# Optimization experiments

Measured on AMD Instinct MI355X. Metric: run time of the kernel, lower is better.

Reference implementation:

```python
import jax, jax.numpy as jnp
import numpy as np

N_HEADS = 16
D_K = 64
DIM = 1024
NEG = -1e12
LN_EPS = 1e-5


def setup_inputs() -> dict:
    key = jax.random.key(0)
    ks = jax.random.split(key, 8)
    B, S, D = 2, 2048, DIM
    H, K = N_HEADS, D_K
    f = lambda k, shp: jax.random.normal(k, shp, dtype=jnp.float32)
    scale = 0.02
    return {
        "input_Q": f(ks[0], (B, S, D)),
        "input_K": f(ks[1], (B, S, D)),
        "input_V": f(ks[2], (B, S, D)),
        "attention_mask": jax.random.randint(ks[3], (B, S), 0, 2, dtype=jnp.int32),
        "W_Q": f(ks[4], (H * K, D)) * scale,  # nn.Linear weight layout [out, in]
        "W_K": f(ks[5], (H * K, D)) * scale,
        "W_V": f(ks[6], (H * K, D)) * scale,
        "W_O": f(ks[7], (D, H * K)) * scale,
        "gamma": jnp.ones((D,), jnp.float32),
        "beta": jnp.zeros((D,), jnp.float32),
    }


def reference(input_Q, input_K, input_V, attention_mask, W_Q, W_K, W_V, W_O, gamma, beta):
    B, S, D = input_Q.shape

    def proj(x, W):  # [B,S,D] @ [HK,D]^T -> [B,H,S,K]
        return (x @ W.T).reshape(B, S, N_HEADS, D_K).transpose(0, 2, 1, 3)

    Q = proj(input_Q, W_Q)
    K = proj(input_K, W_K)
    V = proj(input_V, W_V)

    scores = jnp.einsum('bhqk,bhsk->bhqs', Q, K) / np.float32(np.sqrt(D_K))

    # Faithful reproduction of scores_mask (including its inverted-looking logic):
    # mask = clamp(padding_mask + strict_upper_tri - 1, min=0); scores += (1-mask)*NEG
    am = attention_mask.astype(scores.dtype)[:, None, None, :]          # [B,1,1,S]
    low_tri = jnp.triu(jnp.ones((S, S), scores.dtype), k=1)             # 1 - tril(ones)
    m = jnp.maximum(am + low_tri - 1.0, 0.0)
    scores = scores + (1.0 - m) * NEG

    attn = jax.nn.softmax(scores, axis=-1)
    ctx = jnp.einsum('bhqs,bhsk->bhqk', attn, V)                        # [B,H,S,K]
    ctx = ctx.transpose(0, 2, 1, 3).reshape(B, S, N_HEADS * D_K)

    out = ctx @ W_O.T + input_Q                                         # fc + residual
    mu = jnp.mean(out, axis=-1, keepdims=True)
    var = jnp.var(out, axis=-1, keepdims=True)
    return (out - mu) / jnp.sqrt(var + LN_EPS) * gamma + beta
```

## Files before the change

### kernel.cpp

```cpp
#include <hip/hip_runtime.h>

#define NH    16
#define DK    64
#define DIM   1024
#define BATCH 2
#define SEQ   2048
#define MROWS (BATCH*SEQ)
#define QSCALE 0.18033688011112043f
#define SENT   -44.0f
#define PCONST 5.684341886080802e-14f

typedef unsigned short bfraw;
typedef __attribute__((ext_vector_type(8))) __bf16 bf16x8;
typedef __attribute__((ext_vector_type(4))) __bf16 bf16x4;
typedef __attribute__((ext_vector_type(8))) unsigned short u16x8;
typedef __attribute__((ext_vector_type(4))) unsigned short u16x4;
typedef __attribute__((ext_vector_type(4))) short s16x4;
typedef __attribute__((ext_vector_type(4))) float f32x4;

__device__ __forceinline__ float bf2f(bfraw u) {
    union { unsigned int i; float f; } x; x.i = ((unsigned int)u) << 16; return x.f;
}
__device__ __forceinline__ bfraw f2bf(float f) {
    union { float f; unsigned int i; } x; x.f = f;
    unsigned int r = x.i + 0x7FFFu + ((x.i >> 16) & 1u);
    return (bfraw)(r >> 16);
}
__device__ __forceinline__ bfraw f2bf_trunc(float f) {
    union { float f; unsigned int i; } x; x.f = f;
    return (bfraw)(x.i >> 16);
}
__device__ __forceinline__ float fexp2(float x) {
#if __has_builtin(__builtin_amdgcn_exp2f)
    return __builtin_amdgcn_exp2f(x);
#else
    return exp2f(x);
#endif
}

__device__ __forceinline__ f32x4 mfma16(s16x4 a, s16x4 b, f32x4 c) {
#if __has_builtin(__builtin_amdgcn_mfma_f32_16x16x16_bf16)
    union { s16x4 s; bf16x4 h; } ua, ub; ua.s = a; ub.s = b;
    return __builtin_amdgcn_mfma_f32_16x16x16_bf16(ua.h, ub.h, c, 0, 0, 0);
#elif __has_builtin(__builtin_amdgcn_mfma_f32_16x16x16bf16_1k)
    return __builtin_amdgcn_mfma_f32_16x16x16bf16_1k(a, b, c, 0, 0, 0);
#else
    asm("v_mfma_f32_16x16x16_bf16 %0, %1, %2, %0" : "+v"(c) : "v"(a), "v"(b));
    return c;
#endif
}

__device__ __forceinline__ float block_reduce(float val, float* rbuf, int op) {
    const int lane = threadIdx.x & 63, wave = threadIdx.x >> 6;
    #pragma unroll
    for (int off = 32; off; off >>= 1) {
        float o = __shfl_xor(val, off, 64);
        val = op ? (val + o) : fmaxf(val, o);
    }
    if (lane == 0) rbuf[wave] = val;
    __syncthreads();
    float r = op ? (rbuf[0] + rbuf[1] + rbuf[2] + rbuf[3])
                 : fmaxf(fmaxf(rbuf[0], rbuf[1]), fmaxf(rbuf[2], rbuf[3]));
    __syncthreads();
    return r;
}

__global__ __launch_bounds__(256) void cvt_kernel(
        const float* __restrict__ x0, const float* __restrict__ x1, const float* __restrict__ x2,
        const float* __restrict__ w0, const float* __restrict__ w1, const float* __restrict__ w2,
        const float* __restrict__ w3, bfraw* __restrict__ Xb, bfraw* __restrict__ Wb) {
    const int t = blockIdx.y;
    const float* src; bfraw* dst; int n;
    if (t < 3) { src = (t == 0) ? x0 : (t == 1) ? x1 : x2; dst = Xb + t * (MROWS * DIM); n = MROWS * DIM; }
    else { int u = t - 3; src = (u == 0) ? w0 : (u == 1) ? w1 : (u == 2) ? w2 : w3;
           dst = Wb + u * (DIM * DIM); n = DIM * DIM; }
    int idx = (blockIdx.x * 256 + threadIdx.x) * 8;
    if (idx >= n) return;
    f32x4 a = *(const f32x4*)(src + idx);
    f32x4 b = *(const f32x4*)(src + idx + 4);
    u16x8 o;
    #pragma unroll
    for (int j = 0; j < 4; j++) { o[j] = f2bf(a[j]); o[4 + j] = f2bf(b[j]); }
    *(u16x8*)(dst + idx) = o;
}

__device__ __forceinline__ void gemm128(const bfraw* __restrict__ A, const bfraw* __restrict__ B,
                                        int m0, int n0, f32x4 acc[4][4]) {
    __shared__ __align__(16) bfraw As[128 * 64];
    __shared__ __align__(16) bfraw Bs[128 * 64];
    const int tid = threadIdx.x, wave = tid >> 6;
    const int lane = tid & 63, lrow = lane & 15, quad = lane >> 4;
    const int wy = wave >> 1, wx = wave & 1;
    const int swz = lrow & 7;
    const int srow = tid >> 2;
    const int cg0  = (tid & 3) << 1;
    const int gc   = cg0 << 3;
    const int e7   = srow & 7;
    const int o0 = ((cg0 ^ e7) << 3), o1 = (((cg0 | 1) ^ e7) << 3);

    u16x8 ha[4], hb[4];
    const bfraw* pa0 = A + (m0 + srow) * DIM + gc;
    const bfraw* pa1 = A + (m0 + 64 + srow) * DIM + gc;
    const bfraw* pb0 = B + (n0 + srow) * DIM + gc;
    const bfraw* pb1 = B + (n0 + 64 + srow) * DIM + gc;

    #pragma unroll
    for (int i = 0; i < 4; i++)
        #pragma unroll
        for (int j = 0; j < 4; j++) { f32x4 z = {0.f, 0.f, 0.f, 0.f}; acc[i][j] = z; }

    ha[0] = *(const u16x8*)(pa0);     ha[1] = *(const u16x8*)(pa0 + 8);
    ha[2] = *(const u16x8*)(pa1);     ha[3] = *(const u16x8*)(pa1 + 8);
    hb[0] = *(const u16x8*)(pb0);     hb[1] = *(const u16x8*)(pb0 + 8);
    hb[2] = *(const u16x8*)(pb1);     hb[3] = *(const u16x8*)(pb1 + 8);

    for (int k0 = 0; k0 < DIM; k0 += 64) {
        __syncthreads();
        *(u16x8*)&As[srow * 64 + o0]        = ha[0];
        *(u16x8*)&As[srow * 64 + o1]        = ha[1];
        *(u16x8*)&As[(64 + srow) * 64 + o0] = ha[2];
        *(u16x8*)&As[(64 + srow) * 64 + o1] = ha[3];
        *(u16x8*)&Bs[srow * 64 + o0]        = hb[0];
        *(u16x8*)&Bs[srow * 64 + o1]        = hb[1];
        *(u16x8*)&Bs[(64 + srow) * 64 + o0] = hb[2];
        *(u16x8*)&Bs[(64 + srow) * 64 + o1] = hb[3];
        __syncthreads();
        if (k0 + 64 < DIM) {
            const int k1 = k0 + 64;
            ha[0] = *(const u16x8*)(pa0 + k1);     ha[1] = *(const u16x8*)(pa0 + k1 + 8);
            ha[2] = *(const u16x8*)(pa1 + k1);     ha[3] = *(const u16x8*)(pa1 + k1 + 8);
            hb[0] = *(const u16x8*)(pb0 + k1);     hb[1] = *(const u16x8*)(pb0 + k1 + 8);
            hb[2] = *(const u16x8*)(pb1 + k1);     hb[3] = *(const u16x8*)(pb1 + k1 + 8);
        }
        #pragma unroll
        for (int ks = 0; ks < 2; ks++) {
            const int c = (ks << 2) | quad;
            bf16x8 af[4], bfg[4];
            #pragma unroll
            for (int mi = 0; mi < 4; mi++)
                af[mi] = *(const bf16x8*)&As[(wy * 64 + mi * 16 + lrow) * 64 + ((c ^ swz) << 3)];
            #pragma unroll
            for (int ni = 0; ni < 4; ni++)
                bfg[ni] = *(const bf16x8*)&Bs[(wx * 64 + ni * 16 + lrow) * 64 + ((c ^ swz) << 3)];
            #pragma unroll
            for (int mi = 0; mi < 4; mi++)
                #pragma unroll
                for (int ni = 0; ni < 4; ni++)
                    acc[mi][ni] = __builtin_amdgcn_mfma_f32_16x16x32_bf16(af[mi], bfg[ni], acc[mi][ni], 0, 0, 0);
        }
    }
}

__global__ __launch_bounds__(256) void qkv_gemm(
        const bfraw* __restrict__ Xb, const bfraw* __restrict__ Wb,
        bfraw* __restrict__ Qp, bfraw* __restrict__ Kp, bfraw* __restrict__ Vt) {
    const int which = blockIdx.z;
    const bfraw* A = Xb + which * (MROWS * DIM);
    const bfraw* B = Wb + which * (DIM * DIM);
    bfraw* O = (which == 0) ? Qp : (which == 1) ? Kp : Vt;
    const int m0 = blockIdx.x * 128, n0 = blockIdx.y * 128;
    f32x4 acc[4][4];
    gemm128(A, B, m0, n0, acc);
    const int lane = threadIdx.x & 63, wave = threadIdx.x >> 6;
    const int lrow = lane & 15, quad = lane >> 4;
    const int wy = wave >> 1, wx = wave & 1;
    const float scale = (which == 0) ? QSCALE : 1.0f;
    #pragma unroll
    for (int mi = 0; mi < 4; mi++)
        #pragma unroll
        for (int ni = 0; ni < 4; ni++)
            #pragma unroll
            for (int i = 0; i < 4; i++) {
                int m = m0 + wy * 64 + mi * 16 + quad * 4 + i;
                int n = n0 + wx * 64 + ni * 16 + lrow;
                int b = m >> 11, s = m & (SEQ - 1), h = n >> 6, kk = n & (DK - 1);
                bfraw v = f2bf(acc[mi][ni][i] * scale);
                if (which == 2) O[(((b * NH + h) * DK) + kk) * SEQ + s] = v;
                else            O[(((b * NH + h) * SEQ) + s) * DK + kk] = v;
            }
}

__global__ __launch_bounds__(256) void vsum_kernel(const bfraw* __restrict__ Vt,
                                                   float* __restrict__ Scum) {
    __shared__ float Ts[32][65];
    const int bh = blockIdx.x, tid = threadIdx.x;
    const int d = tid & 63, part = tid >> 6;
    const bfraw* vrow = Vt + (bh * DK + d) * SEQ;
    for (int qt = part * 8; qt < part * 8 + 8; qt++) {
        float s = 0.f;
        #pragma unroll
        for (int j = 0; j < 64; j += 8) {
            u16x8 v = *(const u16x8*)(vrow + qt * 64 + j);
            #pragma unroll
            for (int e = 0; e < 8; e++) s += bf2f(v[e]);
        }
        Ts[qt][d] = s;
    }
    __syncthreads();
    if (tid < 64) {
        float run = 0.f;
        for (int qt = 0; qt < 32; qt++) {
            Scum[(bh * 32 + qt) * 64 + tid] = run;
            run += Ts[qt][tid];
        }
    }
}

__global__ __launch_bounds__(256) void attn_flash(
        const bfraw* __restrict__ Qp, const bfraw* __restrict__ Kp, const bfraw* __restrict__ Vt,
        const float* __restrict__ Scum, const int* __restrict__ mask, bfraw* __restrict__ Ctx) {
    __shared__ __align__(16) bfraw Ks[2][64 * 64];
    __shared__ __align__(16) bfraw Vs[2][64 * 64];
    __shared__ unsigned short Mk[SEQ];
    const int bh = blockIdx.x, yy = blockIdx.y;
    const int gg = yy >> 3, jj = yy & 7;
    const int qt = (gg == 0) ? jj : (gg == 1) ? (31 - jj) : (gg == 2) ? (8 + jj) : (23 - jj);
    const int b = bh >> 4, h = bh & 15;
    const int tid = threadIdx.x, wave = tid >> 6, lane = tid & 63;
    const int lrow = lane & 15, quad = lane >> 4;
    const int baseK = ((b * NH + h) * SEQ) * DK;
    const int baseV = ((b * NH + h) * DK) * SEQ;
    const int qbase = qt * 64 + wave * 16;
    const int q_ln  = qbase + lrow;
    const int diagKt = qt * 64;
    const int ldr = tid >> 2;
    const int cg0 = (tid & 3) << 1;
    const int ldc = cg0 << 3;
    const int e7 = ldr & 7;
    const int cl0 = ((cg0 ^ e7) << 3), cl1 = (((cg0 | 1) ^ e7) << 3);

    for (int i = tid; i < SEQ; i += 256) Mk[i] = (unsigned short)(mask[b * SEQ + i] != 0);

    bf16x8 qf[2];
    qf[0] = *(const bf16x8*)(Qp + baseK + (qbase + lrow) * DK + quad * 8);
    qf[1] = *(const bf16x8*)(Qp + baseK + (qbase + lrow) * DK + 32 + quad * 8);

    f32x4 Oa[4];
    #pragma unroll
    for (int nd = 0; nd < 4; nd++) {
        f32x4 sv = *(const f32x4*)&Scum[(bh * 32 + qt) * 64 + nd * 16 + quad * 4];
        #pragma unroll
        for (int i = 0; i < 4; i++) Oa[nd][i] = PCONST * sv[i];
    }
    float lsum = 0.f;

    const int nt = (SEQ - diagKt) >> 6;
    int kt0 = diagKt;
    u16x8 k0 = *(const u16x8*)(Kp + baseK + (kt0 + ldr) * DK + ldc);
    u16x8 k1 = *(const u16x8*)(Kp + baseK + (kt0 + ldr) * DK + ldc + 8);
    u16x8 v0 = *(const u16x8*)(Vt + baseV + ldr * SEQ + kt0 + ldc);
    u16x8 v1 = *(const u16x8*)(Vt + baseV + ldr * SEQ + kt0 + ldc + 8);

    for (int t = 0; t < nt; t++, kt0 += 64) {
        bfraw* Kb = Ks[t & 1];
        bfraw* Vb = Vs[t & 1];
        *(u16x8*)&Kb[ldr * 64 + cl0] = k0;
        *(u16x8*)&Kb[ldr * 64 + cl1] = k1;
        *(u16x8*)&Vb[ldr * 64 + cl0] = v0;
        *(u16x8*)&Vb[ldr * 64 + cl1] = v1;
        if (t + 1 < nt) {
            const int kn = kt0 + 64;
            k0 = *(const u16x8*)(Kp + baseK + (kn + ldr) * DK + ldc);
            k1 = *(const u16x8*)(Kp + baseK + (kn + ldr) * DK + ldc + 8);
            v0 = *(const u16x8*)(Vt + baseV + ldr * SEQ + kn + ldc);
            v1 = *(const u16x8*)(Vt + baseV + ldr * SEQ + kn + ldc + 8);
        }
        __syncthreads();

        s16x4 pb[4];
        #pragma unroll
        for (int n = 0; n < 4; n++) {
            const int srow = n * 16 + lrow;
            bf16x8 kfa = *(const bf16x8*)&Kb[srow * 64 + ((quad ^ (lrow & 7)) << 3)];
            bf16x8 kfb = *(const bf16x8*)&Kb[srow * 64 + (((4 | quad) ^ (lrow & 7)) << 3)];
            f32x4 z = {0.f, 0.f, 0.f, 0.f};
            z = __builtin_amdgcn_mfma_f32_16x16x32_bf16(kfa, qf[0], z, 0, 0, 0);
            z = __builtin_amdgcn_mfma_f32_16x16x32_bf16(kfb, qf[1], z, 0, 0, 0);
            u16x4 pu;
            if (t == 0) {
                #pragma unroll
                for (int i = 0; i < 4; i++) {
                    int s = kt0 + n * 16 + quad * 4 + i;
                    bool valid = (Mk[s] != 0) && (s > q_ln);
                    float p = fexp2(valid ? z[i] : SENT);
                    lsum += p; pu[i] = f2bf_trunc(p);
                }
            } else {
                #pragma unroll
                for (int i = 0; i < 4; i++) {
                    int s = kt0 + n * 16 + quad * 4 + i;
                    float p = fexp2(Mk[s] ? z[i] : SENT);
                    lsum += p; pu[i] = f2bf_trunc(p);
                }
            }
            union { u16x4 u; s16x4 s; } cv; cv.u = pu; pb[n] = cv.s;
        }

        #pragma unroll
        for (int nd = 0; nd < 4; nd++) {
            const int d = nd * 16 + lrow;
            #pragma unroll
            for (int sc = 0; sc < 4; sc++) {
                s16x4 vf = *(const s16x4*)&Vb[d * 64
                    + ((((sc << 1) | (quad >> 1)) ^ (d & 7)) << 3) + ((quad & 1) << 2)];
                Oa[nd] = mfma16(vf, pb[sc], Oa[nd]);
            }
        }
    }

    float r = lsum;
    r += __shfl_xor(r, 16, 64);
    r += __shfl_xor(r, 32, 64);
    const float inv = 1.0f / (r + (float)diagKt * PCONST);
    #pragma unroll
    for (int nd = 0; nd < 4; nd++) {
        u16x4 o;
        #pragma unroll
        for (int i = 0; i < 4; i++) o[i] = f2bf(Oa[nd][i] * inv);
        *(u16x4*)&Ctx[(b * SEQ + q_ln) * DIM + h * DK + nd * 16 + quad * 4] = o;
    }
}

__global__ __launch_bounds__(256) void out_gemm(
        const bfraw* __restrict__ Ctx, const bfraw* __restrict__ WoB, float* __restrict__ C) {
    const int m0 = blockIdx.x * 128, n0 = blockIdx.y * 128;
    f32x4 acc[4][4];
    gemm128(Ctx, WoB, m0, n0, acc);
    const int lane = threadIdx.x & 63, wave = threadIdx.x >> 6;
    const int lrow = lane & 15, quad = lane >> 4;
    const int wy = wave >> 1, wx = wave & 1;
    #pragma unroll
    for (int mi = 0; mi < 4; mi++)
        #pragma unroll
        for (int ni = 0; ni < 4; ni++)
            #pragma unroll
            for (int i = 0; i < 4; i++) {
                int m = m0 + wy * 64 + mi * 16 + quad * 4 + i;
                int n = n0 + wx * 64 + ni * 16 + lrow;
                C[m * DIM + n] = acc[mi][ni][i];
            }
}

__global__ __launch_bounds__(256) void ln_kernel(
        const float* __restrict__ C, const float* __restrict__ Xq,
        const float* __restrict__ gamma, const float* __restrict__ beta,
        float* __restrict__ out) {
    __shared__ float rbuf[4];
    const int m = blockIdx.x, tid = threadIdx.x;
    const float* crow = C + m * DIM;
    const float* xrow = Xq + m * DIM;
    float v[4]; float s = 0.f, s2 = 0.f;
    #pragma unroll
    for (int i = 0; i < 4; i++) {
        int d = tid + (i << 8);
        float x = crow[d] + xrow[d];
        v[i] = x; s += x; s2 += x * x;
    }
    float S  = block_reduce(s,  rbuf, 1);
    float S2 = block_reduce(s2, rbuf, 1);
    float mu  = S * (1.0f / DIM);
    float var = S2 * (1.0f / DIM) - mu * mu;
    float rstd = rsqrtf(var + 1e-5f);
    #pragma unroll
    for (int i = 0; i < 4; i++) {
        int d = tid + (i << 8);
        out[m * DIM + d] = (v[i] - mu) * rstd * gamma[d] + beta[d];
    }
}

extern "C" void kernel_launch(void* const* d_in, const int* in_sizes, int n_in,
                              void* d_out, int out_size, void* d_ws, size_t ws_size,
                              hipStream_t stream) {
    const float* Xq    = (const float*)d_in[0];
    const float* Xk    = (const float*)d_in[1];
    const float* Xv    = (const float*)d_in[2];
    const int*   mask  = (const int*)  d_in[3];
    const float* Wq    = (const float*)d_in[4];
    const float* Wk    = (const float*)d_in[5];
    const float* Wv    = (const float*)d_in[6];
    const float* Wo    = (const float*)d_in[7];
    const float* gamma = (const float*)d_in[8];
    const float* beta  = (const float*)d_in[9];
    float* out = (float*)d_out;

    char* ws = (char*)d_ws;
    bfraw* Xb   = (bfraw*)(ws);
    bfraw* Wb   = (bfraw*)(ws + (24u << 20));
    bfraw* Qp   = (bfraw*)(ws + (32u << 20));
    bfraw* Kp   = (bfraw*)(ws + (40u << 20));
    bfraw* Vt   = (bfraw*)(ws + (48u << 20));
    bfraw* Ctx  = (bfraw*)(ws + (56u << 20));
    float* C    = (float*)(ws);
    float* Scum = (float*)(ws + (16u << 20));

    dim3 blk(256);
    cvt_kernel<<<dim3(MROWS * DIM / (256 * 8), 7), blk, 0, stream>>>(Xq, Xk, Xv, Wq, Wk, Wv, Wo, Xb, Wb);
    qkv_gemm  <<<dim3(MROWS / 128, DIM / 128, 3),  blk, 0, stream>>>(Xb, Wb, Qp, Kp, Vt);
    vsum_kernel<<<dim3(BATCH * NH),                blk, 0, stream>>>(Vt, Scum);
    attn_flash<<<dim3(BATCH * NH, SEQ / 64),       blk, 0, stream>>>(Qp, Kp, Vt, Scum, mask, Ctx);
    out_gemm  <<<dim3(MROWS / 128, DIM / 128),     blk, 0, stream>>>(Ctx, Wb + 3 * (DIM * DIM), C);
    ln_kernel <<<dim3(MROWS),                      blk, 0, stream>>>(C, Xq, gamma, beta, out);
}
```

Measured before the change: 227.6 us.

## Load GEMM tiles directly global-to-LDS with global_load_lds, dropping register staging

Replaces the register-staged global loads and LDS stores in the shared 128x128 GEMM tile loop with direct global-to-LDS 16-byte loads. The XOR swizzle moves to the global column address so the LDS layout stays compatible with the existing fragment reads. This frees VGPRs and removes the LDS store instructions. It also drops the software prefetch of the next k-tile, so loads are no longer overlapped with the MFMA work of the previous tile, and the barrier may not wait for the asynchronous LDS writes without an explicit vmcnt wait.

```diff
diff --git a/kernel.cpp b/kernel.cpp
--- a/kernel.cpp
+++ b/kernel.cpp
@@ -48,6 +48,12 @@
     asm("v_mfma_f32_16x16x16_bf16 %0, %1, %2, %0" : "+v"(c) : "v"(a), "v"(b));
     return c;
 #endif
+}
+
+__device__ __forceinline__ void gl2lds16(const bfraw* g, bfraw* l) {
+    __builtin_amdgcn_global_load_lds(
+        (const __attribute__((address_space(1))) void*)g,
+        (__attribute__((address_space(3))) void*)l, 16, 0, 0);
 }
 
 __device__ __forceinline__ float block_reduce(float val, float* rbuf, int op) {
@@ -92,46 +98,28 @@
     const int lane = tid & 63, lrow = lane & 15, quad = lane >> 4;
     const int wy = wave >> 1, wx = wave & 1;
     const int swz = lrow & 7;
-    const int srow = tid >> 2;
-    const int cg0  = (tid & 3) << 1;
-    const int gc   = cg0 << 3;
-    const int e7   = srow & 7;
-    const int o0 = ((cg0 ^ e7) << 3), o1 = (((cg0 | 1) ^ e7) << 3);
-
-    u16x8 ha[4], hb[4];
-    const bfraw* pa0 = A + (m0 + srow) * DIM + gc;
-    const bfraw* pa1 = A + (m0 + 64 + srow) * DIM + gc;
-    const bfraw* pb0 = B + (n0 + srow) * DIM + gc;
-    const bfraw* pb1 = B + (n0 + 64 + srow) * DIM + gc;
+
+    const int srow = lane >> 3;
+    const int cpos = lane & 7;
+    const int gcol = ((cpos ^ srow) << 3);
+    const bfraw* gA = A + (m0 + wave * 8 + srow) * DIM + gcol;
+    const bfraw* gB = B + (n0 + wave * 8 + srow) * DIM + gcol;
+    bfraw* lA = &As[wave * 512];
+    bfraw* lB = &Bs[wave * 512];
 
     #pragma unroll
     for (int i = 0; i < 4; i++)
         #pragma unroll
         for (int j = 0; j < 4; j++) { f32x4 z = {0.f, 0.f, 0.f, 0.f}; acc[i][j] = z; }
-
-    ha[0] = *(const u16x8*)(pa0);     ha[1] = *(const u16x8*)(pa0 + 8);
-    ha[2] = *(const u16x8*)(pa1);     ha[3] = *(const u16x8*)(pa1 + 8);
-    hb[0] = *(const u16x8*)(pb0);     hb[1] = *(const u16x8*)(pb0 + 8);
-    hb[2] = *(const u16x8*)(pb1);     hb[3] = *(const u16x8*)(pb1 + 8);
 
     for (int k0 = 0; k0 < DIM; k0 += 64) {
         __syncthreads();
-        *(u16x8*)&As[srow * 64 + o0]        = ha[0];
-        *(u16x8*)&As[srow * 64 + o1]        = ha[1];
-        *(u16x8*)&As[(64 + srow) * 64 + o0] = ha[2];
-        *(u16x8*)&As[(64 + srow) * 64 + o1] = ha[3];
-        *(u16x8*)&Bs[srow * 64 + o0]        = hb[0];
-        *(u16x8*)&Bs[srow * 64 + o1]        = hb[1];
-        *(u16x8*)&Bs[(64 + srow) * 64 + o0] = hb[2];
-        *(u16x8*)&Bs[(64 + srow) * 64 + o1] = hb[3];
+        #pragma unroll
+        for (int i = 0; i < 4; i++) {
+            gl2lds16(gA + i * 32 * DIM + k0, lA + i * 2048);
+            gl2lds16(gB + i * 32 * DIM + k0, lB + i * 2048);
+        }
         __syncthreads();
-        if (k0 + 64 < DIM) {
-            const int k1 = k0 + 64;
-            ha[0] = *(const u16x8*)(pa0 + k1);     ha[1] = *(const u16x8*)(pa0 + k1 + 8);
-            ha[2] = *(const u16x8*)(pa1 + k1);     ha[3] = *(const u16x8*)(pa1 + k1 + 8);
-            hb[0] = *(const u16x8*)(pb0 + k1);     hb[1] = *(const u16x8*)(pb0 + k1 + 8);
-            hb[2] = *(const u16x8*)(pb1 + k1);     hb[3] = *(const u16x8*)(pb1 + k1 + 8);
-        }
         #pragma unroll
         for (int ks = 0; ks < 2; ks++) {
             const int c = (ks << 2) | quad;
```

Measured after the change: 232.7 us. +2.2%, slower.

## Double-buffer shared-memory tiles and prefetch two k-steps ahead in GEMM

Applied to the files above, without the earlier changes.

The bf16 GEMM core now uses two LDS buffers for the A and B tiles and keeps two register prefetch stages, loading global data two 64-wide k-steps ahead. Each step needs one barrier instead of two, and the k loop is fully unrolled. The aim is to hide global-load latency and barrier stalls behind the MFMA work. In exchange the kernel uses twice the LDS (64 KB per block) and more VGPRs, which may lower occupancy.

```diff
diff --git a/kernel.cpp b/kernel.cpp
--- a/kernel.cpp
+++ b/kernel.cpp
@@ -86,8 +86,8 @@
 
 __device__ __forceinline__ void gemm128(const bfraw* __restrict__ A, const bfraw* __restrict__ B,
                                         int m0, int n0, f32x4 acc[4][4]) {
-    __shared__ __align__(16) bfraw As[128 * 64];
-    __shared__ __align__(16) bfraw Bs[128 * 64];
+    __shared__ __align__(16) bfraw As[2][128 * 64];
+    __shared__ __align__(16) bfraw Bs[2][128 * 64];
     const int tid = threadIdx.x, wave = tid >> 6;
     const int lane = tid & 63, lrow = lane & 15, quad = lane >> 4;
     const int wy = wave >> 1, wx = wave & 1;
@@ -98,7 +98,6 @@
     const int e7   = srow & 7;
     const int o0 = ((cg0 ^ e7) << 3), o1 = (((cg0 | 1) ^ e7) << 3);
 
-    u16x8 ha[4], hb[4];
     const bfraw* pa0 = A + (m0 + srow) * DIM + gc;
     const bfraw* pa1 = A + (m0 + 64 + srow) * DIM + gc;
     const bfraw* pb0 = B + (n0 + srow) * DIM + gc;
@@ -109,45 +108,57 @@
         #pragma unroll
         for (int j = 0; j < 4; j++) { f32x4 z = {0.f, 0.f, 0.f, 0.f}; acc[i][j] = z; }
 
-    ha[0] = *(const u16x8*)(pa0);     ha[1] = *(const u16x8*)(pa0 + 8);
-    ha[2] = *(const u16x8*)(pa1);     ha[3] = *(const u16x8*)(pa1 + 8);
-    hb[0] = *(const u16x8*)(pb0);     hb[1] = *(const u16x8*)(pb0 + 8);
-    hb[2] = *(const u16x8*)(pb1);     hb[3] = *(const u16x8*)(pb1 + 8);
-
-    for (int k0 = 0; k0 < DIM; k0 += 64) {
-        __syncthreads();
-        *(u16x8*)&As[srow * 64 + o0]        = ha[0];
-        *(u16x8*)&As[srow * 64 + o1]        = ha[1];
-        *(u16x8*)&As[(64 + srow) * 64 + o0] = ha[2];
-        *(u16x8*)&As[(64 + srow) * 64 + o1] = ha[3];
-        *(u16x8*)&Bs[srow * 64 + o0]        = hb[0];
-        *(u16x8*)&Bs[srow * 64 + o1]        = hb[1];
-        *(u16x8*)&Bs[(64 + srow) * 64 + o0] = hb[2];
-        *(u16x8*)&Bs[(64 + srow) * 64 + o1] = hb[3];
-        __syncthreads();
-        if (k0 + 64 < DIM) {
-            const int k1 = k0 + 64;
-            ha[0] = *(const u16x8*)(pa0 + k1);     ha[1] = *(const u16x8*)(pa0 + k1 + 8);
-            ha[2] = *(const u16x8*)(pa1 + k1);     ha[3] = *(const u16x8*)(pa1 + k1 + 8);
-            hb[0] = *(const u16x8*)(pb0 + k1);     hb[1] = *(const u16x8*)(pb0 + k1 + 8);
-            hb[2] = *(const u16x8*)(pb1 + k1);     hb[3] = *(const u16x8*)(pb1 + k1 + 8);
-        }
+    u16x8 ha0[4], hb0[4], ha1[4], hb1[4];
+
+    auto LOAD = [&](u16x8 ha[4], u16x8 hb[4], int kk) {
+        ha[0] = *(const u16x8*)(pa0 + kk);     ha[1] = *(const u16x8*)(pa0 + kk + 8);
+        ha[2] = *(const u16x8*)(pa1 + kk);     ha[3] = *(const u16x8*)(pa1 + kk + 8);
+        hb[0] = *(const u16x8*)(pb0 + kk);     hb[1] = *(const u16x8*)(pb0 + kk + 8);
+        hb[2] = *(const u16x8*)(pb1 + kk);     hb[3] = *(const u16x8*)(pb1 + kk + 8);
+    };
+    auto STORE = [&](bfraw* Ad, bfraw* Bd, u16x8 ha[4], u16x8 hb[4]) {
+        *(u16x8*)&Ad[srow * 64 + o0]        = ha[0];
+        *(u16x8*)&Ad[srow * 64 + o1]        = ha[1];
+        *(u16x8*)&Ad[(64 + srow) * 64 + o0] = ha[2];
+        *(u16x8*)&Ad[(64 + srow) * 64 + o1] = ha[3];
+        *(u16x8*)&Bd[srow * 64 + o0]        = hb[0];
+        *(u16x8*)&Bd[srow * 64 + o1]        = hb[1];
+        *(u16x8*)&Bd[(64 + srow) * 64 + o0] = hb[2];
+        *(u16x8*)&Bd[(64 + srow) * 64 + o1] = hb[3];
+    };
+    auto COMPUTE = [&](const bfraw* Ad, const bfraw* Bd) {
         #pragma unroll
         for (int ks = 0; ks < 2; ks++) {
             const int c = (ks << 2) | quad;
             bf16x8 af[4], bfg[4];
             #pragma unroll
             for (int mi = 0; mi < 4; mi++)
-                af[mi] = *(const bf16x8*)&As[(wy * 64 + mi * 16 + lrow) * 64 + ((c ^ swz) << 3)];
+                af[mi] = *(const bf16x8*)&Ad[(wy * 64 + mi * 16 + lrow) * 64 + ((c ^ swz) << 3)];
             #pragma unroll
             for (int ni = 0; ni < 4; ni++)
-                bfg[ni] = *(const bf16x8*)&Bs[(wx * 64 + ni * 16 + lrow) * 64 + ((c ^ swz) << 3)];
+                bfg[ni] = *(const bf16x8*)&Bd[(wx * 64 + ni * 16 + lrow) * 64 + ((c ^ swz) << 3)];
             #pragma unroll
             for (int mi = 0; mi < 4; mi++)
                 #pragma unroll
                 for (int ni = 0; ni < 4; ni++)
                     acc[mi][ni] = __builtin_amdgcn_mfma_f32_16x16x32_bf16(af[mi], bfg[ni], acc[mi][ni], 0, 0, 0);
         }
+    };
+
+    LOAD(ha0, hb0, 0);
+    LOAD(ha1, hb1, 64);
+
+    #pragma unroll
+    for (int m2 = 0; m2 < DIM / 128; m2++) {
+        const int k0 = m2 * 128;
+        STORE(As[0], Bs[0], ha0, hb0);
+        if (k0 + 128 < DIM) LOAD(ha0, hb0, k0 + 128);
+        __syncthreads();
+        COMPUTE(As[0], Bs[0]);
+        STORE(As[1], Bs[1], ha1, hb1);
+        if (k0 + 192 < DIM) LOAD(ha1, hb1, k0 + 192);
+        __syncthreads();
+        COMPUTE(As[1], Bs[1]);
     }
 }
 
```

Result: no change. 224.0 us (-1.6%).
